# Performance work log

Measured on AMD Instinct MI355X. Metric: run time of the kernel, lower is better.

The kernel has to match this reference:

```python
import jax, jax.numpy as jnp
import numpy as np

B, H, W, C = 128, 256, 256, 3  # per init_kwargs input_shape (batch resolved to 128)


def setup_inputs() -> dict:
    key = jax.random.key(0)
    inputs = jax.random.normal(key, (B, 6 + H * W * C), dtype=jnp.float32)
    return {"inputs": inputs}


def reference(inputs):
    # Split flat input into affine params and image (NHWC)
    theta = inputs[:, :6].reshape(-1, 2, 3)                 # (B, 2, 3)
    image = inputs[:, 6:].reshape(-1, H, W, C)              # (B, H, W, C)

    # --- affine grid generation over the INPUT spatial size ---
    xt, yt = jnp.meshgrid(
        jnp.linspace(-1.0, 1.0, W, dtype=inputs.dtype),
        jnp.linspace(-1.0, 1.0, H, dtype=inputs.dtype),
    )                                                        # each (H, W)
    ones = jnp.ones_like(xt)
    grid = jnp.stack([xt.ravel(), yt.ravel(), ones.ravel()])  # (3, H*W) homogeneous
    batch_grids = jnp.einsum('bij,jp->bip', theta, grid)      # (B, 2, H*W)
    batch_grids = batch_grids.reshape(-1, 2, H, W)
    x_s = batch_grids[:, 0]                                   # (B, H, W) in [-1, 1]
    y_s = batch_grids[:, 1]

    # --- bilinear sampling ---
    max_x, max_y = W - 1, H - 1
    x = 0.5 * (x_s + 1.0) * max_x                             # rescale to pixel coords
    y = 0.5 * (y_s + 1.0) * max_y

    x0 = jnp.floor(x).astype(jnp.int32)
    x1 = x0 + 1
    y0 = jnp.floor(y).astype(jnp.int32)
    y1 = y0 + 1

    x0 = jnp.clip(x0, 0, max_x)
    x1 = jnp.clip(x1, 0, max_x)
    y0 = jnp.clip(y0, 0, max_y)
    y1 = jnp.clip(y1, 0, max_y)

    b = jnp.arange(image.shape[0])[:, None, None]             # (B, 1, 1)
    Ia = image[b, y0, x0]                                     # (B, H, W, C)
    Ib = image[b, y1, x0]
    Ic = image[b, y0, x1]
    Id = image[b, y1, x1]

    # weights from CLIPPED corner coords (matches TF STN reference impl)
    x0f = x0.astype(x.dtype); x1f = x1.astype(x.dtype)
    y0f = y0.astype(y.dtype); y1f = y1.astype(y.dtype)
    wa = ((x1f - x) * (y1f - y))[..., None]
    wb = ((x1f - x) * (y - y0f))[..., None]
    wc = ((x - x0f) * (y1f - y))[..., None]
    wd = ((x - x0f) * (y - y0f))[..., None]

    return wa * Ia + wb * Ib + wc * Ic + wd * Id              # (B, H, W, C)
```

## Files before the change

### kernel.cpp

```cpp
#include <hip/hip_runtime.h>


constexpr int BB = 128;
constexpr int HH = 256;
constexpr int WW = 256;
constexpr int CC = 3;
constexpr long long IMG_ELEMS = (long long)HH * WW * CC;
constexpr long long ROW_ELEMS = 6 + IMG_ELEMS;
constexpr int NWG = BB * 32;
constexpr int LDSW = 98;

typedef float f32x4 __attribute__((ext_vector_type(4)));
typedef float f32x2 __attribute__((ext_vector_type(2)));
typedef f32x4 f32x4_a4 __attribute__((aligned(4)));
typedef f32x2 f32x2_a4 __attribute__((aligned(4)));
struct F3 { float v[3]; };

__device__ __forceinline__ void sample_px(
    const float* __restrict__ img,
    float t00, float t01, float t02, float t10, float t11, float t12,
    int w, int h, float o[3])
{
    const float xt = -1.0f + (2.0f / (WW - 1)) * (float)w;
    const float yt = -1.0f + (2.0f / (HH - 1)) * (float)h;
    const float x_s = t00 * xt + t01 * yt + t02;
    const float y_s = t10 * xt + t11 * yt + t12;
    const float x = 0.5f * (x_s + 1.0f) * (float)(WW - 1);
    const float y = 0.5f * (y_s + 1.0f) * (float)(HH - 1);

    const int x0 = (int)floorf(x);
    const int y0 = (int)floorf(y);
    const int x0c = min(max(x0,     0), WW - 1);
    const int x1c = min(max(x0 + 1, 0), WW - 1);
    const int y0c = min(max(y0,     0), HH - 1);
    const int y1c = min(max(y0 + 1, 0), HH - 1);
    const int xp  = min(max(x0, 0), WW - 2);

    const float* plo = img + (y0c * WW + xp) * CC;
    const float* phi = img + (y1c * WW + xp) * CC;
    const f32x4_a4 lo4 = *reinterpret_cast<const f32x4_a4*>(plo);
    const f32x2_a4 lo2 = *reinterpret_cast<const f32x2_a4*>(plo + 4);
    const f32x4_a4 hi4 = *reinterpret_cast<const f32x4_a4*>(phi);
    const f32x2_a4 hi2 = *reinterpret_cast<const f32x2_a4*>(phi + 4);

    const float loP0[3] = {lo4.x, lo4.y, lo4.z};
    const float loP1[3] = {lo4.w, lo2.x, lo2.y};
    const float hiP0[3] = {hi4.x, hi4.y, hi4.z};
    const float hiP1[3] = {hi4.w, hi2.x, hi2.y};

    const bool selA = (x0 > WW - 2);
    const bool selC = (x0 >= 0);

    const float x0f = (float)x0c, x1f = (float)x1c;
    const float y0f = (float)y0c, y1f = (float)y1c;
    const float wa = (x1f - x) * (y1f - y);
    const float wb = (x1f - x) * (y - y0f);
    const float wc = (x - x0f) * (y1f - y);
    const float wd = (x - x0f) * (y - y0f);

    #pragma unroll
    for (int c = 0; c < 3; ++c) {
        const float Ia = selA ? loP1[c] : loP0[c];
        const float Ib = selA ? hiP1[c] : hiP0[c];
        const float Ic = selC ? loP1[c] : loP0[c];
        const float Id = selC ? hiP1[c] : hiP0[c];
        o[c] = wa * Ia + wb * Ib + wc * Ic + wd * Id;
    }
}

__global__ __launch_bounds__(256) void bilinear_sampler_kernel(
    const float* __restrict__ in, float* __restrict__ out)
{
    __shared__ float lds[64 * LDSW];

    const int bid = blockIdx.x;
    const int swz = (bid & 7) * (NWG >> 3) + (bid >> 3);
    const int b    = swz >> 5;
    const int beta = swz & 31;

    const float* __restrict__ base = in + (long long)b * ROW_ELEMS;
    const float t00 = base[0], t01 = base[1], t02 = base[2];
    const float t10 = base[3], t11 = base[4], t12 = base[5];
    const float* __restrict__ img = base + 6;
    float* __restrict__ outb = out + (long long)b * IMG_ELEMS;

    const int tid = threadIdx.x;

    if (fabsf(t10) <= fabsf(t11)) {
        const int h0 = beta * 8;
        const int w  = tid;
        #pragma unroll
        for (int r = 0; r < 8; ++r) {
            float o[3];
            sample_px(img, t00, t01, t02, t10, t11, t12, w, h0 + r, o);
            F3 s; s.v[0] = o[0]; s.v[1] = o[1]; s.v[2] = o[2];
            *reinterpret_cast<F3*>(outb + ((h0 + r) * WW + w) * CC) = s;
        }
    } else {
        const int h0 = (beta & 3) * 64;
        const int w0 = (beta >> 2) * 32;
        const int l  = tid & 63;
        const int v  = tid >> 6;
        #pragma unroll
        for (int j = 0; j < 8; ++j) {
            const int c = v * 8 + j;
            float o[3];
            sample_px(img, t00, t01, t02, t10, t11, t12, w0 + c, h0 + l, o);
            float* dst = &lds[l * LDSW + c * 3];
            dst[0] = o[0]; dst[1] = o[1]; dst[2] = o[2];
        }
        __syncthreads();
        #pragma unroll
        for (int p = 0; p < 12; ++p) {
            const int d2 = p * 256 + tid;
            const int r  = d2 / 48;
            const int k  = d2 % 48;
            const f32x2 val = *reinterpret_cast<const f32x2*>(&lds[r * LDSW + k * 2]);
            *reinterpret_cast<f32x2*>(outb + (h0 + r) * (WW * CC) + w0 * CC + k * 2) = val;
        }
    }
}

extern "C" void kernel_launch(void* const* d_in, const int* in_sizes, int n_in,
                              void* d_out, int out_size, void* d_ws, size_t ws_size,
                              hipStream_t stream)
{
    const float* in = (const float*)d_in[0];
    float* out = (float*)d_out;
    dim3 grid(NWG), block(256);
    bilinear_sampler_kernel<<<grid, block, 0, stream>>>(in, out);
}
```

Before: 41.48 us.

## Split each bilinear sample across lane pairs and combine with shuffles

```diff
diff --git a/kernel.cpp b/kernel.cpp
--- a/kernel.cpp
+++ b/kernel.cpp
@@ -10,17 +10,21 @@
 constexpr int NWG = BB * 32;
 constexpr int LDSW = 98;
 
-typedef float f32x4 __attribute__((ext_vector_type(4)));
 typedef float f32x2 __attribute__((ext_vector_type(2)));
-typedef f32x4 f32x4_a4 __attribute__((aligned(4)));
-typedef f32x2 f32x2_a4 __attribute__((aligned(4)));
 struct F3 { float v[3]; };
 
-__device__ __forceinline__ void sample_px(
-    const float* __restrict__ img,
+struct SCoord {
+    int ylo, yhi;
+    int col0, col1;
+    float wlo0, whi0;
+    float wlo1, whi1;
+};
+
+__device__ __forceinline__ SCoord make_scoord(
     float t00, float t01, float t02, float t10, float t11, float t12,
-    int w, int h, float o[3])
+    int w, int h)
 {
+    SCoord q;
     const float xt = -1.0f + (2.0f / (WW - 1)) * (float)w;
     const float yt = -1.0f + (2.0f / (HH - 1)) * (float)h;
     const float x_s = t00 * xt + t01 * yt + t02;
@@ -30,41 +34,32 @@
 
     const int x0 = (int)floorf(x);
     const int y0 = (int)floorf(y);
-    const int x0c = min(max(x0,     0), WW - 1);
-    const int x1c = min(max(x0 + 1, 0), WW - 1);
-    const int y0c = min(max(y0,     0), HH - 1);
-    const int y1c = min(max(y0 + 1, 0), HH - 1);
-    const int xp  = min(max(x0, 0), WW - 2);
+    q.col0 = min(max(x0,     0), WW - 1);
+    q.col1 = min(max(x0 + 1, 0), WW - 1);
+    q.ylo  = min(max(y0,     0), HH - 1);
+    q.yhi  = min(max(y0 + 1, 0), HH - 1);
 
-    const float* plo = img + (y0c * WW + xp) * CC;
-    const float* phi = img + (y1c * WW + xp) * CC;
-    const f32x4_a4 lo4 = *reinterpret_cast<const f32x4_a4*>(plo);
-    const f32x2_a4 lo2 = *reinterpret_cast<const f32x2_a4*>(plo + 4);
-    const f32x4_a4 hi4 = *reinterpret_cast<const f32x4_a4*>(phi);
-    const f32x2_a4 hi2 = *reinterpret_cast<const f32x2_a4*>(phi + 4);
+    const float x0f = (float)q.col0, x1f = (float)q.col1;
+    const float y0f = (float)q.ylo,  y1f = (float)q.yhi;
+    q.wlo0 = (x1f - x) * (y1f - y);
+    q.whi0 = (x1f - x) * (y - y0f);
+    q.wlo1 = (x - x0f) * (y1f - y);
+    q.whi1 = (x - x0f) * (y - y0f);
+    return q;
+}
 
-    const float loP0[3] = {lo4.x, lo4.y, lo4.z};
-    const float loP1[3] = {lo4.w, lo2.x, lo2.y};
-    const float hiP0[3] = {hi4.x, hi4.y, hi4.z};
-    const float hiP1[3] = {hi4.w, hi2.x, hi2.y};
-
-    const bool selA = (x0 > WW - 2);
-    const bool selC = (x0 >= 0);
-
-    const float x0f = (float)x0c, x1f = (float)x1c;
-    const float y0f = (float)y0c, y1f = (float)y1c;
-    const float wa = (x1f - x) * (y1f - y);
-    const float wb = (x1f - x) * (y - y0f);
-    const float wc = (x - x0f) * (y1f - y);
-    const float wd = (x - x0f) * (y - y0f);
-
+__device__ __forceinline__ void pair_sample(
+    const float* __restrict__ img, const SCoord& q, int odd, float o[3])
+{
+    const int mycol = odd ? q.col1 : q.col0;
+    const float wlo = odd ? q.wlo1 : q.wlo0;
+    const float whi = odd ? q.whi1 : q.whi0;
+    const F3 vlo = *reinterpret_cast<const F3*>(img + (q.ylo * WW + mycol) * CC);
+    const F3 vhi = *reinterpret_cast<const F3*>(img + (q.yhi * WW + mycol) * CC);
     #pragma unroll
     for (int c = 0; c < 3; ++c) {
-        const float Ia = selA ? loP1[c] : loP0[c];
-        const float Ib = selA ? hiP1[c] : hiP0[c];
-        const float Ic = selC ? loP1[c] : loP0[c];
-        const float Id = selC ? hiP1[c] : hiP0[c];
-        o[c] = wa * Ia + wb * Ib + wc * Ic + wd * Id;
+        const float part = wlo * vlo.v[c] + whi * vhi.v[c];
+        o[c] = part + __shfl_xor(part, 1, 64);
     }
 }
 
@@ -85,29 +80,40 @@
     float* __restrict__ outb = out + (long long)b * IMG_ELEMS;
 
     const int tid = threadIdx.x;
+    const int v   = tid >> 6;
+    const int l   = tid & 63;
+    const int i   = l >> 1;
+    const int odd = l & 1;
 
     if (fabsf(t10) <= fabsf(t11)) {
         const int h0 = beta * 8;
-        const int w  = tid;
-        #pragma unroll
-        for (int r = 0; r < 8; ++r) {
+        #pragma unroll 2
+        for (int f = 0; f < 16; ++f) {
+            const int row = h0 + 2 * v + (f >> 3);
+            const int wpx = ((f & 7) << 5) + i;
+            const SCoord q = make_scoord(t00, t01, t02, t10, t11, t12, wpx, row);
             float o[3];
-            sample_px(img, t00, t01, t02, t10, t11, t12, w, h0 + r, o);
-            F3 s; s.v[0] = o[0]; s.v[1] = o[1]; s.v[2] = o[2];
-            *reinterpret_cast<F3*>(outb + ((h0 + r) * WW + w) * CC) = s;
+            pair_sample(img, q, odd, o);
+            if (!odd) {
+                F3 s; s.v[0] = o[0]; s.v[1] = o[1]; s.v[2] = o[2];
+                *reinterpret_cast<F3*>(outb + (row * WW + wpx) * CC) = s;
+            }
         }
     } else {
         const int h0 = (beta & 3) * 64;
         const int w0 = (beta >> 2) * 32;
-        const int l  = tid & 63;
-        const int v  = tid >> 6;
-        #pragma unroll
-        for (int j = 0; j < 8; ++j) {
-            const int c = v * 8 + j;
+        #pragma unroll 2
+        for (int f = 0; f < 16; ++f) {
+            const int cpx  = 8 * v + (f >> 1);
+            const int hloc = ((f & 1) << 5) + i;
+            const SCoord q = make_scoord(t00, t01, t02, t10, t11, t12,
+                                         w0 + cpx, h0 + hloc);
             float o[3];
-            sample_px(img, t00, t01, t02, t10, t11, t12, w0 + c, h0 + l, o);
-            float* dst = &lds[l * LDSW + c * 3];
-            dst[0] = o[0]; dst[1] = o[1]; dst[2] = o[2];
+            pair_sample(img, q, odd, o);
+            if (!odd) {
+                float* dst = &lds[hloc * LDSW + cpx * 3];
+                dst[0] = o[0]; dst[1] = o[1]; dst[2] = o[2];
+            }
         }
         __syncthreads();
         #pragma unroll
@@ -116,7 +122,8 @@
             const int r  = d2 / 48;
             const int k  = d2 % 48;
             const f32x2 val = *reinterpret_cast<const f32x2*>(&lds[r * LDSW + k * 2]);
-            *reinterpret_cast<f32x2*>(outb + (h0 + r) * (WW * CC) + w0 * CC + k * 2) = val;
+            *reinterpret_cast<f32x2*>(
+                outb + (h0 + r) * (WW * CC) + w0 * CC + k * 2) = val;
         }
     }
 }
```

Measured after the change: 38.79 us. 6.5% less time.
